# Performance work log

Measured on AMD Instinct MI355X. Metric: run time of the kernel, lower is better.

## Reference

```python
import jax, jax.numpy as jnp
import numpy as np

N = 500000      # data points
D = 64          # n_in
NS = 128        # N_samples


def setup_inputs() -> dict:
    key = jax.random.key(0)
    k1, k2, k3, k4 = jax.random.split(key, 4)
    X = jax.random.normal(k1, (N, D), dtype=jnp.float32)
    w_mu = jax.random.normal(k2, (D,), dtype=jnp.float32)
    w_log_var = jax.random.normal(k3, (D,), dtype=jnp.float32)
    z = jax.random.normal(k4, (NS,), dtype=jnp.float32)  # z_i samples
    return {"X": X, "w_mu": w_mu, "w_log_var": w_log_var, "z": z}


def reference(X, w_mu, w_log_var, z):
    # mean_i = X @ w_mu                       [N]
    mean_i = X @ w_mu
    # std_i = sqrt(diag(X diag(exp(lv)) X^T)) == sqrt(sum_j X_ij^2 * exp(lv_j))
    var_i = jnp.einsum('nd,d->n', X * X, jnp.exp(w_log_var))  # [N]
    std_i = jnp.sqrt(var_i)
    # activation_mat[i, s] = std_i * z_s + mean_i          [N, NS]
    activation_mat = std_i[:, None] * z[None, :] + mean_i[:, None]
    return jax.nn.sigmoid(activation_mat)
```

## Files before the change

### kernel.cpp

```cpp
#include <hip/hip_runtime.h>
#include <math.h>


typedef float f4 __attribute__((ext_vector_type(4)));

__device__ __forceinline__ f4 sigmoid4(float s2, float m2, f4 zz) {
    f4 r;
    r.x = __builtin_amdgcn_rcpf(1.0f + __builtin_amdgcn_exp2f(fmaf(zz.x, s2, m2)));
    r.y = __builtin_amdgcn_rcpf(1.0f + __builtin_amdgcn_exp2f(fmaf(zz.y, s2, m2)));
    r.z = __builtin_amdgcn_rcpf(1.0f + __builtin_amdgcn_exp2f(fmaf(zz.z, s2, m2)));
    r.w = __builtin_amdgcn_rcpf(1.0f + __builtin_amdgcn_exp2f(fmaf(zz.w, s2, m2)));
    return r;
}

__global__ __launch_bounds__(256) void logreg_sample_kernel(
    const float* __restrict__ X,
    const float* __restrict__ w_mu,
    const float* __restrict__ w_lv,
    const float* __restrict__ z,
    float* __restrict__ out,
    int n_rows)
{
    const int tid = blockIdx.x * blockDim.x + threadIdx.x;
    const int grp = tid >> 4;
    const int l   = tid & 15;
    const int r0  = grp * 4;
    if (r0 >= n_rows) return;

    const f4 mu4 = ((const f4*)w_mu)[l];
    const f4 lv4 = ((const f4*)w_lv)[l];
    f4 ev4;
    ev4.x = __expf(lv4.x); ev4.y = __expf(lv4.y);
    ev4.z = __expf(lv4.z); ev4.w = __expf(lv4.w);
    const f4 z0 = ((const f4*)z)[l];
    const f4 z1 = ((const f4*)z)[16 + l];

    const f4* X4 = (const f4*)X;
    const int nfull = (r0 + 4 <= n_rows) ? 4 : (n_rows - r0);

    if (__builtin_expect(nfull == 4, 1)) {
        f4 x[4];
        #pragma unroll
        for (int j = 0; j < 4; ++j)
            x[j] = __builtin_nontemporal_load(&X4[(size_t)(r0 + j) * 16 + l]);

        float a[4], b[4];
        #pragma unroll
        for (int j = 0; j < 4; ++j) {
            a[j] = x[j].x * mu4.x + x[j].y * mu4.y + x[j].z * mu4.z + x[j].w * mu4.w;
            b[j] = x[j].x * x[j].x * ev4.x + x[j].y * x[j].y * ev4.y
                 + x[j].z * x[j].z * ev4.z + x[j].w * x[j].w * ev4.w;
        }

        #pragma unroll
        for (int m = 1; m < 16; m <<= 1) {
            #pragma unroll
            for (int j = 0; j < 4; ++j) {
                a[j] += __shfl_xor(a[j], m, 64);
                b[j] += __shfl_xor(b[j], m, 64);
            }
        }

        const float NEG_LOG2E = -1.4426950408889634f;
        #pragma unroll
        for (int j = 0; j < 4; ++j) {
            const float s2 = sqrtf(b[j]) * NEG_LOG2E;
            const float m2 = a[j] * NEG_LOG2E;
            f4* orow = (f4*)(out + (size_t)(r0 + j) * 128);
            __builtin_nontemporal_store(sigmoid4(s2, m2, z0), &orow[l]);
            __builtin_nontemporal_store(sigmoid4(s2, m2, z1), &orow[16 + l]);
        }
    } else {
        for (int j = 0; j < nfull; ++j) {
            f4 x = X4[(size_t)(r0 + j) * 16 + l];
            float a = x.x * mu4.x + x.y * mu4.y + x.z * mu4.z + x.w * mu4.w;
            float b = x.x * x.x * ev4.x + x.y * x.y * ev4.y
                    + x.z * x.z * ev4.z + x.w * x.w * ev4.w;
            for (int m = 1; m < 16; m <<= 1) {
                a += __shfl_xor(a, m, 64);
                b += __shfl_xor(b, m, 64);
            }
            const float NEG_LOG2E = -1.4426950408889634f;
            const float s2 = sqrtf(b) * NEG_LOG2E;
            const float m2 = a * NEG_LOG2E;
            f4* orow = (f4*)(out + (size_t)(r0 + j) * 128);
            __builtin_nontemporal_store(sigmoid4(s2, m2, z0), &orow[l]);
            __builtin_nontemporal_store(sigmoid4(s2, m2, z1), &orow[16 + l]);
        }
    }
}

extern "C" void kernel_launch(void* const* d_in, const int* in_sizes, int n_in,
                              void* d_out, int out_size, void* d_ws, size_t ws_size,
                              hipStream_t stream) {
    const float* X    = (const float*)d_in[0];
    const float* w_mu = (const float*)d_in[1];
    const float* w_lv = (const float*)d_in[2];
    const float* z    = (const float*)d_in[3];
    float* out = (float*)d_out;

    const int n_rows   = in_sizes[0] / 64;
    const int n_groups = (n_rows + 3) / 4;
    const int threads  = n_groups * 16;
    const int blocks   = (threads + 255) / 256;

    logreg_sample_kernel<<<blocks, 256, 0, stream>>>(X, w_mu, w_lv, z, out, n_rows);
}
```

Before: 334.1 us.

## Stage per-row stats in LDS and write output rows with full-wavefront coalesced stores

Restructures the kernel into two phases per 64-row block. First, 16-lane groups reduce the mean and std for each row and write them to shared memory. After a barrier, each 32-lane half-wave writes one full 512-byte output row, so every store instruction covers contiguous rows. The goal is better coalescing of the output write, which dominates traffic, at the cost of a block barrier and LDS reads.

```diff
diff --git a/kernel.cpp b/kernel.cpp
--- a/kernel.cpp
+++ b/kernel.cpp
@@ -4,16 +4,9 @@
 
 typedef float f4 __attribute__((ext_vector_type(4)));
 
-__device__ __forceinline__ f4 sigmoid4(float s2, float m2, f4 zz) {
-    f4 r;
-    r.x = __builtin_amdgcn_rcpf(1.0f + __builtin_amdgcn_exp2f(fmaf(zz.x, s2, m2)));
-    r.y = __builtin_amdgcn_rcpf(1.0f + __builtin_amdgcn_exp2f(fmaf(zz.y, s2, m2)));
-    r.z = __builtin_amdgcn_rcpf(1.0f + __builtin_amdgcn_exp2f(fmaf(zz.z, s2, m2)));
-    r.w = __builtin_amdgcn_rcpf(1.0f + __builtin_amdgcn_exp2f(fmaf(zz.w, s2, m2)));
-    return r;
-}
+#define RPB 64
 
-__global__ __launch_bounds__(256) void logreg_sample_kernel(
+__global__ __launch_bounds__(256) void logreg_fused(
     const float* __restrict__ X,
     const float* __restrict__ w_mu,
     const float* __restrict__ w_lv,
@@ -21,37 +14,41 @@
     float* __restrict__ out,
     int n_rows)
 {
-    const int tid = blockIdx.x * blockDim.x + threadIdx.x;
-    const int grp = tid >> 4;
-    const int l   = tid & 15;
+    __shared__ float s_m2[RPB];
+    __shared__ float s_s2[RPB];
+
+    const float NEG_LOG2E = -1.4426950408889634f;
+    const int t    = threadIdx.x;
+    const int row0 = blockIdx.x * RPB;
+    const int nblk = min(RPB, n_rows - row0);
+
+    const int grp = t >> 4;
+    const int l   = t & 15;
     const int r0  = grp * 4;
-    if (r0 >= n_rows) return;
 
     const f4 mu4 = ((const f4*)w_mu)[l];
     const f4 lv4 = ((const f4*)w_lv)[l];
     f4 ev4;
     ev4.x = __expf(lv4.x); ev4.y = __expf(lv4.y);
     ev4.z = __expf(lv4.z); ev4.w = __expf(lv4.w);
-    const f4 z0 = ((const f4*)z)[l];
-    const f4 z1 = ((const f4*)z)[16 + l];
 
     const f4* X4 = (const f4*)X;
-    const int nfull = (r0 + 4 <= n_rows) ? 4 : (n_rows - r0);
 
-    if (__builtin_expect(nfull == 4, 1)) {
+    if (__builtin_expect(nblk == RPB, 1)) {
         f4 x[4];
         #pragma unroll
         for (int j = 0; j < 4; ++j)
-            x[j] = __builtin_nontemporal_load(&X4[(size_t)(r0 + j) * 16 + l]);
+            x[j] = __builtin_nontemporal_load(
+                &X4[(size_t)(row0 + r0 + j) * 16 + l]);
 
         float a[4], b[4];
         #pragma unroll
         for (int j = 0; j < 4; ++j) {
-            a[j] = x[j].x * mu4.x + x[j].y * mu4.y + x[j].z * mu4.z + x[j].w * mu4.w;
+            a[j] = x[j].x * mu4.x + x[j].y * mu4.y
+                 + x[j].z * mu4.z + x[j].w * mu4.w;
             b[j] = x[j].x * x[j].x * ev4.x + x[j].y * x[j].y * ev4.y
                  + x[j].z * x[j].z * ev4.z + x[j].w * x[j].w * ev4.w;
         }
-
         #pragma unroll
         for (int m = 1; m < 16; m <<= 1) {
             #pragma unroll
@@ -60,32 +57,51 @@
                 b[j] += __shfl_xor(b[j], m, 64);
             }
         }
-
-        const float NEG_LOG2E = -1.4426950408889634f;
-        #pragma unroll
-        for (int j = 0; j < 4; ++j) {
-            const float s2 = sqrtf(b[j]) * NEG_LOG2E;
-            const float m2 = a[j] * NEG_LOG2E;
-            f4* orow = (f4*)(out + (size_t)(r0 + j) * 128);
-            __builtin_nontemporal_store(sigmoid4(s2, m2, z0), &orow[l]);
-            __builtin_nontemporal_store(sigmoid4(s2, m2, z1), &orow[16 + l]);
+        if (l == 0) {
+            #pragma unroll
+            for (int j = 0; j < 4; ++j) {
+                s_m2[r0 + j] = a[j] * NEG_LOG2E;
+                s_s2[r0 + j] = sqrtf(b[j]) * NEG_LOG2E;
+            }
         }
     } else {
-        for (int j = 0; j < nfull; ++j) {
-            f4 x = X4[(size_t)(r0 + j) * 16 + l];
-            float a = x.x * mu4.x + x.y * mu4.y + x.z * mu4.z + x.w * mu4.w;
-            float b = x.x * x.x * ev4.x + x.y * x.y * ev4.y
-                    + x.z * x.z * ev4.z + x.w * x.w * ev4.w;
-            for (int m = 1; m < 16; m <<= 1) {
-                a += __shfl_xor(a, m, 64);
-                b += __shfl_xor(b, m, 64);
+        for (int j = 0; j < 4; ++j) {
+            const int lr = r0 + j;
+            if (lr < nblk) {
+                f4 x = X4[(size_t)(row0 + lr) * 16 + l];
+                float a = x.x * mu4.x + x.y * mu4.y + x.z * mu4.z + x.w * mu4.w;
+                float b = x.x * x.x * ev4.x + x.y * x.y * ev4.y
+                        + x.z * x.z * ev4.z + x.w * x.w * ev4.w;
+                for (int m = 1; m < 16; m <<= 1) {
+                    a += __shfl_xor(a, m, 64);
+                    b += __shfl_xor(b, m, 64);
+                }
+                if (l == 0) {
+                    s_m2[lr] = a * NEG_LOG2E;
+                    s_s2[lr] = sqrtf(b) * NEG_LOG2E;
+                }
             }
-            const float NEG_LOG2E = -1.4426950408889634f;
-            const float s2 = sqrtf(b) * NEG_LOG2E;
-            const float m2 = a * NEG_LOG2E;
-            f4* orow = (f4*)(out + (size_t)(r0 + j) * 128);
-            __builtin_nontemporal_store(sigmoid4(s2, m2, z0), &orow[l]);
-            __builtin_nontemporal_store(sigmoid4(s2, m2, z1), &orow[16 + l]);
+        }
+    }
+    __syncthreads();
+
+    const int qcol  = t & 31;
+    const int rbase = t >> 5;
+    const f4 zc = ((const f4*)z)[qcol];
+    f4* outb = (f4*)(out + (size_t)row0 * 128);
+
+    #pragma unroll
+    for (int k = 0; k < 8; ++k) {
+        const int lr = rbase + 8 * k;
+        if (lr < nblk) {
+            const float s2 = s_s2[lr];
+            const float m2 = s_m2[lr];
+            f4 o;
+            o.x = __builtin_amdgcn_rcpf(1.0f + __builtin_amdgcn_exp2f(fmaf(zc.x, s2, m2)));
+            o.y = __builtin_amdgcn_rcpf(1.0f + __builtin_amdgcn_exp2f(fmaf(zc.y, s2, m2)));
+            o.z = __builtin_amdgcn_rcpf(1.0f + __builtin_amdgcn_exp2f(fmaf(zc.z, s2, m2)));
+            o.w = __builtin_amdgcn_rcpf(1.0f + __builtin_amdgcn_exp2f(fmaf(zc.w, s2, m2)));
+            __builtin_nontemporal_store(o, &outb[(size_t)lr * 32 + qcol]);
         }
     }
 }
@@ -99,10 +115,8 @@
     const float* z    = (const float*)d_in[3];
     float* out = (float*)d_out;
 
-    const int n_rows   = in_sizes[0] / 64;
-    const int n_groups = (n_rows + 3) / 4;
-    const int threads  = n_groups * 16;
-    const int blocks   = (threads + 255) / 256;
+    const int n_rows = in_sizes[0] / 64;
+    const int blocks = (n_rows + RPB - 1) / RPB;
 
-    logreg_sample_kernel<<<blocks, 256, 0, stream>>>(X, w_mu, w_lv, z, out, n_rows);
+    logreg_fused<<<blocks, 256, 0, stream>>>(X, w_mu, w_lv, z, out, n_rows);
 }
```

Measured after the change: 336.8 us. Within noise of the previous version (+0.8%).
